# Kernel optimization log

Hardware: AMD Instinct MI355X
Metric: run time of the kernel (lower is better)

## Reference

```python
import jax, jax.numpy as jnp
import numpy as np

DIM = 64  # scaling dim from __init__


def setup_inputs() -> dict:
    key = jax.random.key(0)
    kq, kk, kv = jax.random.split(key, 3)
    B, N, D = 16, 2048, 64
    Q = jax.random.normal(kq, (B, N, D), dtype=jnp.float32)
    K = jax.random.normal(kk, (B, N, D), dtype=jnp.float32)
    V = jax.random.normal(kv, (B, N, D), dtype=jnp.float32)
    return {"Q": Q, "K": K, "V": V}


def reference(Q, K, V):
    # Original transposes K to [B, d, N]; the E/F Linformer projections are
    # constructed but their application guards are always False, so the math
    # is plain scaled-dot-product attention. Dropout p=0 (eval baseline).
    scale = 1.0 / (DIM ** 0.5)
    QK = jnp.einsum('bnd,bmd->bnm', Q, K) * scale          # [B, N, N]
    attn_weights = jax.nn.softmax(QK, axis=-1)             # [B, N, N]
    out = jnp.einsum('bnm,bmd->bnd', attn_weights, V)      # [B, N, d]
    return out, attn_weights
```

## Files before the change

kernel.cpp:

```cpp
#include <hip/hip_runtime.h>

#define B_  16
#define N_  2048
#define D_  64
#define KT  64
#define NTILES (N_ / KT)
#define SCALE_LOG2 0.18033688011112042f

typedef __attribute__((ext_vector_type(8))) short  frag8;
typedef __attribute__((ext_vector_type(4))) float  floatx4;

union FragU { frag8 fr; unsigned short us[8]; };

__device__ __forceinline__ unsigned short f2bf(float f) {
    unsigned int u = __builtin_bit_cast(unsigned int, f);
    u += 0x7fffu + ((u >> 16) & 1u);
    return (unsigned short)(u >> 16);
}

struct __align__(16) SMem {
    unsigned short Ks[64][72];
    unsigned short Vt[64][72];
    float          Pf[4][16][68];
};

__global__ __launch_bounds__(256, 4) void attn_fused(
    const float* __restrict__ Q, const float* __restrict__ K,
    const float* __restrict__ V, float* __restrict__ out,
    float* __restrict__ attn)
{
    __shared__ SMem sm;

    const int qtile = blockIdx.x;
    const int b     = blockIdx.y;
    const int qbase = qtile * 64;
    const int tid   = threadIdx.x;
    const int w     = tid >> 6;
    const int lane  = tid & 63;
    const int lm    = lane & 15;
    const int quad  = lane >> 4;
    const int q8    = quad * 8;
    const size_t bN = (size_t)b * N_;

    const int srow = tid >> 2;
    const int sc0  = (tid & 3) * 16;
    const int vswz = srow ^ (((sc0 >> 4) & 3) << 3);

    FragU aq0, aq1;
    {
        const float* qp = Q + (bN + qbase + w*16 + lm) * D_;
        float4 f0 = *(const float4*)(qp + q8);
        float4 f1 = *(const float4*)(qp + q8 + 4);
        float4 f2 = *(const float4*)(qp + 32 + q8);
        float4 f3 = *(const float4*)(qp + 36 + q8);
        #pragma unroll
        for (int j = 0; j < 4; ++j) {
            aq0.us[j]   = f2bf(f0[j]);  aq0.us[4+j] = f2bf(f1[j]);
            aq1.us[j]   = f2bf(f2[j]);  aq1.us[4+j] = f2bf(f3[j]);
        }
    }

    float s4[4] = {0.f, 0.f, 0.f, 0.f};

    ushort4 kreg[4];
    {
        const float4* src = (const float4*)(K + (bN + srow) * D_ + sc0);
        #pragma unroll
        for (int i = 0; i < 4; ++i) {
            float4 f = src[i];
            kreg[i].x=f2bf(f.x); kreg[i].y=f2bf(f.y); kreg[i].z=f2bf(f.z); kreg[i].w=f2bf(f.w);
        }
    }

    for (int t = 0; t < NTILES; ++t) {
        __syncthreads();
        #pragma unroll
        for (int i = 0; i < 4; ++i)
            *(ushort4*)&sm.Ks[srow][sc0 + i*4] = kreg[i];
        __syncthreads();

        float4 fnext[4];
        if (t+1 < NTILES) {
            const float4* src = (const float4*)(K + (bN + (t+1)*KT + srow) * D_ + sc0);
            #pragma unroll
            for (int i = 0; i < 4; ++i) fnext[i] = src[i];
        }

        #pragma unroll
        for (int ns = 0; ns < 4; ++ns) {
            frag8 b0 = *(const frag8*)&sm.Ks[ns*16 + lm][q8];
            frag8 b1 = *(const frag8*)&sm.Ks[ns*16 + lm][32 + q8];
            floatx4 a = {0.f, 0.f, 0.f, 0.f};
            a = __builtin_amdgcn_mfma_f32_16x16x32_bf16(aq0.fr, b0, a, 0, 0, 0);
            a = __builtin_amdgcn_mfma_f32_16x16x32_bf16(aq1.fr, b1, a, 0, 0, 0);
            #pragma unroll
            for (int r = 0; r < 4; ++r)
                s4[r] += exp2f(a[r] * SCALE_LOG2);
        }

        if (t+1 < NTILES) {
            #pragma unroll
            for (int i = 0; i < 4; ++i) {
                kreg[i].x=f2bf(fnext[i].x); kreg[i].y=f2bf(fnext[i].y);
                kreg[i].z=f2bf(fnext[i].z); kreg[i].w=f2bf(fnext[i].w);
            }
        }
    }

    float invl[4];
    #pragma unroll
    for (int r = 0; r < 4; ++r) {
        float v = s4[r];
        #pragma unroll
        for (int off = 1; off < 16; off <<= 1)
            v += __shfl_xor(v, off, 64);
        invl[r] = 1.0f / v;
    }

    floatx4 oacc[4];
    #pragma unroll
    for (int ns = 0; ns < 4; ++ns) oacc[ns] = (floatx4){0.f, 0.f, 0.f, 0.f};

    const int prow = lane >> 3;
    const int pcol = (lane & 7) * 4;

    for (int t = 0; t < NTILES; ++t) {
        __syncthreads();
        {
            const float4* srcK = (const float4*)(K + (bN + t*KT + srow) * D_ + sc0);
            const float4* srcV = (const float4*)(V + (bN + t*KT + srow) * D_ + sc0);
            float4 fk[4], fv[4];
            #pragma unroll
            for (int i = 0; i < 4; ++i) fk[i] = srcK[i];
            #pragma unroll
            for (int i = 0; i < 4; ++i) fv[i] = srcV[i];
            #pragma unroll
            for (int i = 0; i < 4; ++i) {
                ushort4 u; u.x=f2bf(fk[i].x); u.y=f2bf(fk[i].y);
                           u.z=f2bf(fk[i].z); u.w=f2bf(fk[i].w);
                *(ushort4*)&sm.Ks[srow][sc0 + i*4] = u;
            }
            #pragma unroll
            for (int i = 0; i < 4; ++i) {
                sm.Vt[sc0 + i*4 + 0][vswz] = f2bf(fv[i].x);
                sm.Vt[sc0 + i*4 + 1][vswz] = f2bf(fv[i].y);
                sm.Vt[sc0 + i*4 + 2][vswz] = f2bf(fv[i].z);
                sm.Vt[sc0 + i*4 + 3][vswz] = f2bf(fv[i].w);
            }
        }
        __syncthreads();

        floatx4 acc[4];
        #pragma unroll
        for (int ns = 0; ns < 4; ++ns) {
            frag8 b0 = *(const frag8*)&sm.Ks[ns*16 + lm][q8];
            frag8 b1 = *(const frag8*)&sm.Ks[ns*16 + lm][32 + q8];
            floatx4 a = {0.f, 0.f, 0.f, 0.f};
            a = __builtin_amdgcn_mfma_f32_16x16x32_bf16(aq0.fr, b0, a, 0, 0, 0);
            a = __builtin_amdgcn_mfma_f32_16x16x32_bf16(aq1.fr, b1, a, 0, 0, 0);
            acc[ns] = a;
        }

        #pragma unroll
        for (int ns = 0; ns < 4; ++ns)
            #pragma unroll
            for (int r = 0; r < 4; ++r)
                sm.Pf[w][quad*4 + r][ns*16 + lm] =
                    exp2f(acc[ns][r] * SCALE_LOG2) * invl[r];

        #pragma unroll
        for (int rg = 0; rg < 2; ++rg)
            #pragma unroll
            for (int half = 0; half < 2; ++half) {
                float4 pv = *(const float4*)&sm.Pf[w][rg*8 + prow][half*32 + pcol];
                *(float4*)&attn[(bN + qbase + w*16 + rg*8 + prow) * N_
                                + t*KT + half*32 + pcol] = pv;
            }

        FragU pa0, pa1;
        {
            float4 p0 = *(const float4*)&sm.Pf[w][lm][q8];
            float4 p1 = *(const float4*)&sm.Pf[w][lm][q8 + 4];
            float4 p2 = *(const float4*)&sm.Pf[w][lm][32 + q8];
            float4 p3 = *(const float4*)&sm.Pf[w][lm][36 + q8];
            #pragma unroll
            for (int j = 0; j < 4; ++j) {
                pa0.us[j]   = f2bf(p0[j]);  pa0.us[4+j] = f2bf(p1[j]);
                pa1.us[j]   = f2bf(p2[j]);  pa1.us[4+j] = f2bf(p3[j]);
            }
        }

        #pragma unroll
        for (int dg = 0; dg < 4; ++dg) {
            const int kb = q8 ^ (dg << 3);
            frag8 v0 = *(const frag8*)&sm.Vt[dg*16 + lm][kb];
            frag8 v1 = *(const frag8*)&sm.Vt[dg*16 + lm][32 + kb];
            oacc[dg] = __builtin_amdgcn_mfma_f32_16x16x32_bf16(pa0.fr, v0, oacc[dg], 0, 0, 0);
            oacc[dg] = __builtin_amdgcn_mfma_f32_16x16x32_bf16(pa1.fr, v1, oacc[dg], 0, 0, 0);
        }
    }

    #pragma unroll
    for (int dg = 0; dg < 4; ++dg)
        #pragma unroll
        for (int r = 0; r < 4; ++r)
            out[(bN + qbase + w*16 + quad*4 + r) * D_ + dg*16 + lm] = oacc[dg][r];
}

extern "C" void kernel_launch(void* const* d_in, const int* in_sizes, int n_in,
                              void* d_out, int out_size, void* d_ws, size_t ws_size,
                              hipStream_t stream) {
    const float* Q = (const float*)d_in[0];
    const float* K = (const float*)d_in[1];
    const float* V = (const float*)d_in[2];
    float* out  = (float*)d_out;
    float* attn = out + (size_t)B_ * N_ * D_;
    dim3 grid(NTILES, B_);
    attn_fused<<<grid, 256, 0, stream>>>(Q, K, V, out, attn);
}
```

Measured before the change: 375.1 us.

## Double-buffer K/V tiles, load K directly to registers in pass one

The first (row-sum) pass now reads K fragments straight from global memory into registers, with a two-stage register prefetch, and skips LDS and its barriers. The second pass double-buffers the K and Vt LDS tiles so that global loads for the next tile overlap compute, leaving one barrier per iteration instead of two. It also switches to the hardware exp2 intrinsic and the library bf16 conversion, and lowers the launch-bounds occupancy hint from 4 to 2. The costs are more registers, a larger LDS footprint, and possibly lower occupancy.

```diff
diff --git a/kernel.cpp b/kernel.cpp
--- a/kernel.cpp
+++ b/kernel.cpp
@@ -1,4 +1,5 @@
 #include <hip/hip_runtime.h>
+#include <hip/hip_bf16.h>
 
 #define B_  16
 #define N_  2048
@@ -13,18 +14,19 @@
 union FragU { frag8 fr; unsigned short us[8]; };
 
 __device__ __forceinline__ unsigned short f2bf(float f) {
-    unsigned int u = __builtin_bit_cast(unsigned int, f);
-    u += 0x7fffu + ((u >> 16) & 1u);
-    return (unsigned short)(u >> 16);
+    return __builtin_bit_cast(unsigned short, __float2bfloat16(f));
+}
+__device__ __forceinline__ float exp2fast(float x) {
+    return __builtin_amdgcn_exp2f(x);
 }
 
 struct __align__(16) SMem {
-    unsigned short Ks[64][72];
-    unsigned short Vt[64][72];
+    unsigned short Ks[2][64][72];
+    unsigned short Vt[2][64][72];
     float          Pf[4][16][68];
 };
 
-__global__ __launch_bounds__(256, 4) void attn_fused(
+__global__ __launch_bounds__(256, 2) void attn_fused(
     const float* __restrict__ Q, const float* __restrict__ K,
     const float* __restrict__ V, float* __restrict__ out,
     float* __restrict__ attn)
@@ -62,49 +64,43 @@
 
     float s4[4] = {0.f, 0.f, 0.f, 0.f};
 
-    ushort4 kreg[4];
-    {
-        const float4* src = (const float4*)(K + (bN + srow) * D_ + sc0);
-        #pragma unroll
-        for (int i = 0; i < 4; ++i) {
-            float4 f = src[i];
-            kreg[i].x=f2bf(f.x); kreg[i].y=f2bf(f.y); kreg[i].z=f2bf(f.z); kreg[i].w=f2bf(f.w);
-        }
-    }
-
-    for (int t = 0; t < NTILES; ++t) {
-        __syncthreads();
-        #pragma unroll
-        for (int i = 0; i < 4; ++i)
-            *(ushort4*)&sm.Ks[srow][sc0 + i*4] = kreg[i];
-        __syncthreads();
-
-        float4 fnext[4];
-        if (t+1 < NTILES) {
-            const float4* src = (const float4*)(K + (bN + (t+1)*KT + srow) * D_ + sc0);
-            #pragma unroll
-            for (int i = 0; i < 4; ++i) fnext[i] = src[i];
-        }
-
-        #pragma unroll
-        for (int ns = 0; ns < 4; ++ns) {
-            frag8 b0 = *(const frag8*)&sm.Ks[ns*16 + lm][q8];
-            frag8 b1 = *(const frag8*)&sm.Ks[ns*16 + lm][32 + q8];
+    float4 kA[8], kB[8];
+    auto loadKd = [&](float4* kf, int kb) {
+        #pragma unroll
+        for (int ns = 0; ns < 2; ++ns) {
+            const float* base = K + (bN + kb + ns*16 + lm) * D_;
+            kf[ns*4+0] = *(const float4*)(base + q8);
+            kf[ns*4+1] = *(const float4*)(base + q8 + 4);
+            kf[ns*4+2] = *(const float4*)(base + 32 + q8);
+            kf[ns*4+3] = *(const float4*)(base + 36 + q8);
+        }
+    };
+    auto qkStep = [&](const float4* kf) {
+        #pragma unroll
+        for (int ns = 0; ns < 2; ++ns) {
+            FragU c0, c1;
+            #pragma unroll
+            for (int j = 0; j < 4; ++j) {
+                c0.us[j]   = f2bf(kf[ns*4+0][j]);
+                c0.us[4+j] = f2bf(kf[ns*4+1][j]);
+                c1.us[j]   = f2bf(kf[ns*4+2][j]);
+                c1.us[4+j] = f2bf(kf[ns*4+3][j]);
+            }
             floatx4 a = {0.f, 0.f, 0.f, 0.f};
-            a = __builtin_amdgcn_mfma_f32_16x16x32_bf16(aq0.fr, b0, a, 0, 0, 0);
-            a = __builtin_amdgcn_mfma_f32_16x16x32_bf16(aq1.fr, b1, a, 0, 0, 0);
+            a = __builtin_amdgcn_mfma_f32_16x16x32_bf16(aq0.fr, c0.fr, a, 0, 0, 0);
+            a = __builtin_amdgcn_mfma_f32_16x16x32_bf16(aq1.fr, c1.fr, a, 0, 0, 0);
             #pragma unroll
             for (int r = 0; r < 4; ++r)
-                s4[r] += exp2f(a[r] * SCALE_LOG2);
-        }
-
-        if (t+1 < NTILES) {
-            #pragma unroll
-            for (int i = 0; i < 4; ++i) {
-                kreg[i].x=f2bf(fnext[i].x); kreg[i].y=f2bf(fnext[i].y);
-                kreg[i].z=f2bf(fnext[i].z); kreg[i].w=f2bf(fnext[i].w);
-            }
-        }
+                s4[r] += exp2fast(a[r] * SCALE_LOG2);
+        }
+    };
+
+    loadKd(kA, 0);
+    for (int t = 0; t < 64; t += 2) {
+        if (t + 1 < 64) loadKd(kB, (t+1)*32);
+        qkStep(kA);
+        if (t + 2 < 64) loadKd(kA, (t+2)*32);
+        qkStep(kB);
     }
 
     float invl[4];
@@ -124,37 +120,44 @@
     const int prow = lane >> 3;
     const int pcol = (lane & 7) * 4;
 
+    float4 fk[4], fv[4];
+    auto loadS = [&](int t) {
+        const float4* srcK = (const float4*)(K + (bN + t*KT + srow) * D_ + sc0);
+        const float4* srcV = (const float4*)(V + (bN + t*KT + srow) * D_ + sc0);
+        #pragma unroll
+        for (int i = 0; i < 4; ++i) fk[i] = srcK[i];
+        #pragma unroll
+        for (int i = 0; i < 4; ++i) fv[i] = srcV[i];
+    };
+    auto writeS = [&](int buf) {
+        #pragma unroll
+        for (int i = 0; i < 4; ++i) {
+            ushort4 u; u.x=f2bf(fk[i].x); u.y=f2bf(fk[i].y);
+                       u.z=f2bf(fk[i].z); u.w=f2bf(fk[i].w);
+            *(ushort4*)&sm.Ks[buf][srow][sc0 + i*4] = u;
+        }
+        #pragma unroll
+        for (int i = 0; i < 4; ++i) {
+            sm.Vt[buf][sc0 + i*4 + 0][vswz] = f2bf(fv[i].x);
+            sm.Vt[buf][sc0 + i*4 + 1][vswz] = f2bf(fv[i].y);
+            sm.Vt[buf][sc0 + i*4 + 2][vswz] = f2bf(fv[i].z);
+            sm.Vt[buf][sc0 + i*4 + 3][vswz] = f2bf(fv[i].w);
+        }
+    };
+
+    loadS(0);
+    writeS(0);
+    __syncthreads();
+
     for (int t = 0; t < NTILES; ++t) {
-        __syncthreads();
-        {
-            const float4* srcK = (const float4*)(K + (bN + t*KT + srow) * D_ + sc0);
-            const float4* srcV = (const float4*)(V + (bN + t*KT + srow) * D_ + sc0);
-            float4 fk[4], fv[4];
-            #pragma unroll
-            for (int i = 0; i < 4; ++i) fk[i] = srcK[i];
-            #pragma unroll
-            for (int i = 0; i < 4; ++i) fv[i] = srcV[i];
-            #pragma unroll
-            for (int i = 0; i < 4; ++i) {
-                ushort4 u; u.x=f2bf(fk[i].x); u.y=f2bf(fk[i].y);
-                           u.z=f2bf(fk[i].z); u.w=f2bf(fk[i].w);
-                *(ushort4*)&sm.Ks[srow][sc0 + i*4] = u;
-            }
-            #pragma unroll
-            for (int i = 0; i < 4; ++i) {
-                sm.Vt[sc0 + i*4 + 0][vswz] = f2bf(fv[i].x);
-                sm.Vt[sc0 + i*4 + 1][vswz] = f2bf(fv[i].y);
-                sm.Vt[sc0 + i*4 + 2][vswz] = f2bf(fv[i].z);
-                sm.Vt[sc0 + i*4 + 3][vswz] = f2bf(fv[i].w);
-            }
-        }
-        __syncthreads();
+        const int cur = t & 1;
+        if (t + 1 < NTILES) loadS(t + 1);
 
         floatx4 acc[4];
         #pragma unroll
         for (int ns = 0; ns < 4; ++ns) {
-            frag8 b0 = *(const frag8*)&sm.Ks[ns*16 + lm][q8];
-            frag8 b1 = *(const frag8*)&sm.Ks[ns*16 + lm][32 + q8];
+            frag8 b0 = *(const frag8*)&sm.Ks[cur][ns*16 + lm][q8];
+            frag8 b1 = *(const frag8*)&sm.Ks[cur][ns*16 + lm][32 + q8];
             floatx4 a = {0.f, 0.f, 0.f, 0.f};
             a = __builtin_amdgcn_mfma_f32_16x16x32_bf16(aq0.fr, b0, a, 0, 0, 0);
             a = __builtin_amdgcn_mfma_f32_16x16x32_bf16(aq1.fr, b1, a, 0, 0, 0);
@@ -166,7 +169,7 @@
             #pragma unroll
             for (int r = 0; r < 4; ++r)
                 sm.Pf[w][quad*4 + r][ns*16 + lm] =
-                    exp2f(acc[ns][r] * SCALE_LOG2) * invl[r];
+                    exp2fast(acc[ns][r] * SCALE_LOG2) * invl[r];
 
         #pragma unroll
         for (int rg = 0; rg < 2; ++rg)
@@ -193,11 +196,14 @@
         #pragma unroll
         for (int dg = 0; dg < 4; ++dg) {
             const int kb = q8 ^ (dg << 3);
-            frag8 v0 = *(const frag8*)&sm.Vt[dg*16 + lm][kb];
-            frag8 v1 = *(const frag8*)&sm.Vt[dg*16 + lm][32 + kb];
+            frag8 v0 = *(const frag8*)&sm.Vt[cur][dg*16 + lm][kb];
+            frag8 v1 = *(const frag8*)&sm.Vt[cur][dg*16 + lm][32 + kb];
             oacc[dg] = __builtin_amdgcn_mfma_f32_16x16x32_bf16(pa0.fr, v0, oacc[dg], 0, 0, 0);
             oacc[dg] = __builtin_amdgcn_mfma_f32_16x16x32_bf16(pa1.fr, v1, oacc[dg], 0, 0, 0);
         }
+
+        if (t + 1 < NTILES) writeS(cur ^ 1);
+        __syncthreads();
     }
 
     #pragma unroll
```

Measured after the change: 435.6 us. 1.16x slower.

## Split attention into denominator and split-K output kernels with XCD-aware block mapping

Applied to the files above, without the earlier changes.

Splits the fused kernel in two. The first kernel computes softmax denominators over a four-way split of the keys and combines the partial sums with atomics into a workspace. The second kernel splits the keys in half, writes the normalized attention probabilities, and accumulates the output with atomics. Together these raise block count from 512 to 2048 and 1024, map blocks to batches per XCD, software-prefetch K and V one tile ahead, and use the hardware exp2 intrinsic. The cost is two memsets, extra launches, and atomic traffic on the output and denominator buffers.

```diff
diff --git a/kernel.cpp b/kernel.cpp
--- a/kernel.cpp
+++ b/kernel.cpp
@@ -1,10 +1,9 @@
 #include <hip/hip_runtime.h>
+#include <hip/hip_bf16.h>
 
 #define B_  16
 #define N_  2048
 #define D_  64
-#define KT  64
-#define NTILES (N_ / KT)
 #define SCALE_LOG2 0.18033688011112042f
 
 typedef __attribute__((ext_vector_type(8))) short  frag8;
@@ -13,38 +12,37 @@
 union FragU { frag8 fr; unsigned short us[8]; };
 
 __device__ __forceinline__ unsigned short f2bf(float f) {
-    unsigned int u = __builtin_bit_cast(unsigned int, f);
-    u += 0x7fffu + ((u >> 16) & 1u);
-    return (unsigned short)(u >> 16);
-}
-
-struct __align__(16) SMem {
-    unsigned short Ks[64][72];
-    unsigned short Vt[64][72];
-    float          Pf[4][16][68];
-};
-
-__global__ __launch_bounds__(256, 4) void attn_fused(
+    return __builtin_bit_cast(unsigned short, __float2bfloat16(f));
+}
+__device__ __forceinline__ float exp2fast(float x) {
+    return __builtin_amdgcn_exp2f(x);
+}
+
+__global__ __launch_bounds__(256) void denom_kernel(
     const float* __restrict__ Q, const float* __restrict__ K,
-    const float* __restrict__ V, float* __restrict__ out,
-    float* __restrict__ attn)
+    float* __restrict__ ws)
 {
-    __shared__ SMem sm;
-
-    const int qtile = blockIdx.x;
-    const int b     = blockIdx.y;
+    __shared__ unsigned short Ks[64][72];
+
+    const int id    = blockIdx.x;
+    const int xcd   = id & 7;
+    const int s     = id >> 3;
+    const int b     = xcd * 2 + (s >> 7);
+    const int rem   = s & 127;
+    const int qtile = rem >> 2;
+    const int kq    = rem & 3;
     const int qbase = qtile * 64;
-    const int tid   = threadIdx.x;
-    const int w     = tid >> 6;
-    const int lane  = tid & 63;
-    const int lm    = lane & 15;
-    const int quad  = lane >> 4;
-    const int q8    = quad * 8;
+    const int kbase = kq * 512;
     const size_t bN = (size_t)b * N_;
 
+    const int tid  = threadIdx.x;
+    const int w    = tid >> 6;
+    const int lane = tid & 63;
+    const int lm   = lane & 15;
+    const int quad = lane >> 4;
+    const int q8   = quad * 8;
     const int srow = tid >> 2;
     const int sc0  = (tid & 3) * 16;
-    const int vswz = srow ^ (((sc0 >> 4) & 3) << 3);
 
     FragU aq0, aq1;
     {
@@ -64,41 +62,42 @@
 
     ushort4 kreg[4];
     {
-        const float4* src = (const float4*)(K + (bN + srow) * D_ + sc0);
+        const float4* src = (const float4*)(K + (bN + kbase + srow) * D_ + sc0);
         #pragma unroll
         for (int i = 0; i < 4; ++i) {
             float4 f = src[i];
-            kreg[i].x=f2bf(f.x); kreg[i].y=f2bf(f.y); kreg[i].z=f2bf(f.z); kreg[i].w=f2bf(f.w);
-        }
-    }
-
-    for (int t = 0; t < NTILES; ++t) {
+            kreg[i].x=f2bf(f.x); kreg[i].y=f2bf(f.y);
+            kreg[i].z=f2bf(f.z); kreg[i].w=f2bf(f.w);
+        }
+    }
+
+    for (int t = 0; t < 8; ++t) {
         __syncthreads();
         #pragma unroll
         for (int i = 0; i < 4; ++i)
-            *(ushort4*)&sm.Ks[srow][sc0 + i*4] = kreg[i];
+            *(ushort4*)&Ks[srow][sc0 + i*4] = kreg[i];
         __syncthreads();
 
         float4 fnext[4];
-        if (t+1 < NTILES) {
-            const float4* src = (const float4*)(K + (bN + (t+1)*KT + srow) * D_ + sc0);
+        if (t + 1 < 8) {
+            const float4* src = (const float4*)(K + (bN + kbase + (t+1)*64 + srow) * D_ + sc0);
             #pragma unroll
             for (int i = 0; i < 4; ++i) fnext[i] = src[i];
         }
 
         #pragma unroll
         for (int ns = 0; ns < 4; ++ns) {
-            frag8 b0 = *(const frag8*)&sm.Ks[ns*16 + lm][q8];
-            frag8 b1 = *(const frag8*)&sm.Ks[ns*16 + lm][32 + q8];
+            frag8 b0 = *(const frag8*)&Ks[ns*16 + lm][q8];
+            frag8 b1 = *(const frag8*)&Ks[ns*16 + lm][32 + q8];
             floatx4 a = {0.f, 0.f, 0.f, 0.f};
             a = __builtin_amdgcn_mfma_f32_16x16x32_bf16(aq0.fr, b0, a, 0, 0, 0);
             a = __builtin_amdgcn_mfma_f32_16x16x32_bf16(aq1.fr, b1, a, 0, 0, 0);
             #pragma unroll
             for (int r = 0; r < 4; ++r)
-                s4[r] += exp2f(a[r] * SCALE_LOG2);
-        }
-
-        if (t+1 < NTILES) {
+                s4[r] += exp2fast(a[r] * SCALE_LOG2);
+        }
+
+        if (t + 1 < 8) {
             #pragma unroll
             for (int i = 0; i < 4; ++i) {
                 kreg[i].x=f2bf(fnext[i].x); kreg[i].y=f2bf(fnext[i].y);
@@ -107,48 +106,106 @@
         }
     }
 
-    float invl[4];
     #pragma unroll
     for (int r = 0; r < 4; ++r) {
         float v = s4[r];
         #pragma unroll
         for (int off = 1; off < 16; off <<= 1)
             v += __shfl_xor(v, off, 64);
-        invl[r] = 1.0f / v;
-    }
+        if (lm == 0)
+            atomicAdd(&ws[bN + qbase + w*16 + quad*4 + r], v);
+    }
+}
+
+struct __align__(16) SMemB {
+    unsigned short Ks[64][72];
+    unsigned short Vt[64][72];
+    float          Pf[4][16][68];
+};
+
+__global__ __launch_bounds__(256, 4) void attn_kernel(
+    const float* __restrict__ Q, const float* __restrict__ K,
+    const float* __restrict__ V, const float* __restrict__ ws,
+    float* __restrict__ out, float* __restrict__ attn)
+{
+    __shared__ SMemB sm;
+
+    const int id    = blockIdx.x;
+    const int xcd   = id & 7;
+    const int s     = id >> 3;
+    const int b     = xcd * 2 + (s >> 6);
+    const int rem   = s & 63;
+    const int qtile = rem >> 1;
+    const int kh    = rem & 1;
+    const int qbase = qtile * 64;
+    const int kbase = kh * 1024;
+    const size_t bN = (size_t)b * N_;
+
+    const int tid  = threadIdx.x;
+    const int w    = tid >> 6;
+    const int lane = tid & 63;
+    const int lm   = lane & 15;
+    const int quad = lane >> 4;
+    const int q8   = quad * 8;
+    const int srow = tid >> 2;
+    const int sc0  = (tid & 3) * 16;
+    const int vswz = srow ^ (((sc0 >> 4) & 3) << 3);
+
+    FragU aq0, aq1;
+    {
+        const float* qp = Q + (bN + qbase + w*16 + lm) * D_;
+        float4 f0 = *(const float4*)(qp + q8);
+        float4 f1 = *(const float4*)(qp + q8 + 4);
+        float4 f2 = *(const float4*)(qp + 32 + q8);
+        float4 f3 = *(const float4*)(qp + 36 + q8);
+        #pragma unroll
+        for (int j = 0; j < 4; ++j) {
+            aq0.us[j]   = f2bf(f0[j]);  aq0.us[4+j] = f2bf(f1[j]);
+            aq1.us[j]   = f2bf(f2[j]);  aq1.us[4+j] = f2bf(f3[j]);
+        }
+    }
+
+    float invl[4];
+    #pragma unroll
+    for (int r = 0; r < 4; ++r)
+        invl[r] = 1.0f / ws[bN + qbase + w*16 + quad*4 + r];
 
     floatx4 oacc[4];
     #pragma unroll
-    for (int ns = 0; ns < 4; ++ns) oacc[ns] = (floatx4){0.f, 0.f, 0.f, 0.f};
+    for (int dg = 0; dg < 4; ++dg) oacc[dg] = (floatx4){0.f, 0.f, 0.f, 0.f};
 
     const int prow = lane >> 3;
     const int pcol = (lane & 7) * 4;
 
-    for (int t = 0; t < NTILES; ++t) {
-        __syncthreads();
-        {
-            const float4* srcK = (const float4*)(K + (bN + t*KT + srow) * D_ + sc0);
-            const float4* srcV = (const float4*)(V + (bN + t*KT + srow) * D_ + sc0);
-            float4 fk[4], fv[4];
-            #pragma unroll
-            for (int i = 0; i < 4; ++i) fk[i] = srcK[i];
-            #pragma unroll
-            for (int i = 0; i < 4; ++i) fv[i] = srcV[i];
-            #pragma unroll
-            for (int i = 0; i < 4; ++i) {
-                ushort4 u; u.x=f2bf(fk[i].x); u.y=f2bf(fk[i].y);
-                           u.z=f2bf(fk[i].z); u.w=f2bf(fk[i].w);
-                *(ushort4*)&sm.Ks[srow][sc0 + i*4] = u;
-            }
-            #pragma unroll
-            for (int i = 0; i < 4; ++i) {
-                sm.Vt[sc0 + i*4 + 0][vswz] = f2bf(fv[i].x);
-                sm.Vt[sc0 + i*4 + 1][vswz] = f2bf(fv[i].y);
-                sm.Vt[sc0 + i*4 + 2][vswz] = f2bf(fv[i].z);
-                sm.Vt[sc0 + i*4 + 3][vswz] = f2bf(fv[i].w);
-            }
-        }
-        __syncthreads();
+    float4 fk[4], fv[4];
+    auto loadS = [&](int t) {
+        const float4* srcK = (const float4*)(K + (bN + kbase + t*64 + srow) * D_ + sc0);
+        const float4* srcV = (const float4*)(V + (bN + kbase + t*64 + srow) * D_ + sc0);
+        #pragma unroll
+        for (int i = 0; i < 4; ++i) fk[i] = srcK[i];
+        #pragma unroll
+        for (int i = 0; i < 4; ++i) fv[i] = srcV[i];
+    };
+
+    loadS(0);
+    for (int t = 0; t < 16; ++t) {
+        __syncthreads();
+        #pragma unroll
+        for (int i = 0; i < 4; ++i) {
+            ushort4 u; u.x=f2bf(fk[i].x); u.y=f2bf(fk[i].y);
+                       u.z=f2bf(fk[i].z); u.w=f2bf(fk[i].w);
+            *(ushort4*)&sm.Ks[srow][sc0 + i*4] = u;
+        }
+        #pragma unroll
+        for (int i = 0; i < 4; ++i) {
+            sm.Vt[sc0 + i*4 + 0][vswz] = f2bf(fv[i].x);
+            sm.Vt[sc0 + i*4 + 1][vswz] = f2bf(fv[i].y);
+            sm.Vt[sc0 + i*4 + 2][vswz] = f2bf(fv[i].z);
+            sm.Vt[sc0 + i*4 + 3][vswz] = f2bf(fv[i].w);
+        }
+        __syncthreads();
+
+        if (t + 1 < 16) loadS(t + 1);
 
         floatx4 acc[4];
         #pragma unroll
@@ -166,7 +223,7 @@
             #pragma unroll
             for (int r = 0; r < 4; ++r)
                 sm.Pf[w][quad*4 + r][ns*16 + lm] =
-                    exp2f(acc[ns][r] * SCALE_LOG2) * invl[r];
+                    exp2fast(acc[ns][r] * SCALE_LOG2) * invl[r];
 
         #pragma unroll
         for (int rg = 0; rg < 2; ++rg)
@@ -174,7 +231,7 @@
             for (int half = 0; half < 2; ++half) {
                 float4 pv = *(const float4*)&sm.Pf[w][rg*8 + prow][half*32 + pcol];
                 *(float4*)&attn[(bN + qbase + w*16 + rg*8 + prow) * N_
-                                + t*KT + half*32 + pcol] = pv;
+                                + kbase + t*64 + half*32 + pcol] = pv;
             }
 
         FragU pa0, pa1;
@@ -204,7 +261,8 @@
     for (int dg = 0; dg < 4; ++dg)
         #pragma unroll
         for (int r = 0; r < 4; ++r)
-            out[(bN + qbase + w*16 + quad*4 + r) * D_ + dg*16 + lm] = oacc[dg][r];
+            atomicAdd(&out[(bN + qbase + w*16 + quad*4 + r) * D_ + dg*16 + lm],
+                      oacc[dg][r]);
 }
 
 extern "C" void kernel_launch(void* const* d_in, const int* in_sizes, int n_in,
@@ -215,6 +273,10 @@
     const float* V = (const float*)d_in[2];
     float* out  = (float*)d_out;
     float* attn = out + (size_t)B_ * N_ * D_;
-    dim3 grid(NTILES, B_);
-    attn_fused<<<grid, 256, 0, stream>>>(Q, K, V, out, attn);
-}
+    float* ws   = (float*)d_ws;
+
+    hipMemsetAsync(ws, 0, (size_t)B_ * N_ * sizeof(float), stream);
+    hipMemsetAsync(out, 0, (size_t)B_ * N_ * D_ * sizeof(float), stream);
+    denom_kernel<<<dim3(2048), 256, 0, stream>>>(Q, K, ws);
+    attn_kernel <<<dim3(1024), 256, 0, stream>>>(Q, K, V, ws, out, attn);
+}
```

Result: faster. 366.2 us (-2.4%).
